# Kernel optimization log

Measured on AMD Instinct MI355X. Metric: run time of the kernel, lower is better.

Reference implementation:

```python
import jax, jax.numpy as jnp
import numpy as np

B, P, N0 = 8, 32, 10000
K, HIDP = 8, 4
HIDR = 4 * K * HIDP + K   # 136 = backbone output channels
HEADS = 2
E = 160000


def _conv_bn(x, w, b, g, be, dil):
    # x: [B,1,P,N0]; w: [k,1,ks,1]; valid conv along time with dilation dil, then BatchNorm2d (batch stats)
    y = jax.lax.conv_general_dilated(x, w, (1, 1), 'VALID', rhs_dilation=(dil, 1),
                                     dimension_numbers=('NCHW', 'OIHW', 'NCHW'))
    y = y + b[None, :, None, None]
    mu = jnp.mean(y, axis=(0, 2, 3), keepdims=True)
    var = jnp.var(y, axis=(0, 2, 3), keepdims=True)
    return g[None, :, None, None] * (y - mu) * jax.lax.rsqrt(var + 1e-5) + be[None, :, None, None]


def _branch(x, w, b, g, be, dil, pool):
    y = _conv_bn(x, w, b, g, be, dil)
    if pool:  # AdaptiveMaxPool2d((HIDP, N0)): pools only the time axis (node axis already N0)
        T = y.shape[2]
        y = jnp.stack([jnp.max(y[:, :, (i * T) // HIDP: -((-(i + 1) * T) // HIDP), :], axis=2)
                       for i in range(HIDP)], axis=2)
    return y.reshape(y.shape[0], -1, y.shape[-1])  # [B, k*hidP or k, N0]


def _backbone(x, pl1, pl2, pp1, pp2, pg):
    x = x.reshape(-1, 1, P, N0)
    parts = [_branch(x, *pl1, 1, True), _branch(x, *pl2, 1, True),   # local: ks 3,5 dil 1
             _branch(x, *pp1, 2, True), _branch(x, *pp2, 2, True),   # periodic: ks 3,5 dil 2
             _branch(x, *pg, 1, False)]                               # global: ks P, no pool
    return jnp.tanh(jnp.concatenate(parts, axis=1).transpose(0, 2, 1))  # [B, N0, HIDR]


def _gat(xn, W, a_src, a_dst, bias, src, dst, heads, out_ch):
    # PyG GATConv: linear (no bias) -> per-head additive attention -> segment softmax over dst -> scatter-sum
    n = xn.shape[0]
    h = (xn @ W).reshape(n, heads, out_ch)                              # [N,H,C]
    al = jax.nn.leaky_relu(jnp.sum(h * a_src, -1)[src] + jnp.sum(h * a_dst, -1)[dst], 0.2)  # [E',H]
    amax = jax.ops.segment_max(al, dst, num_segments=n)
    ex = jnp.exp(al - amax[dst])
    coef = ex / (jax.ops.segment_sum(ex, dst, num_segments=n)[dst] + 1e-16)
    out = jax.ops.segment_sum(coef[:, :, None] * h[src], dst, num_segments=n)  # [N,H,C]
    return out.reshape(n, heads * out_ch) + bias


def setup_inputs() -> dict:
    key = jax.random.key(0)
    ks = iter(jax.random.split(key, 64))
    nrm = lambda *s: jax.random.normal(next(ks), s, jnp.float32) * 0.05
    d = {"x": jax.random.normal(next(ks), (B, P, N0), jnp.float32)}
    for nm, ksz in (("l1", 3), ("l2", 5), ("p1", 3), ("p2", 5), ("g", P)):
        d["w_" + nm] = nrm(K, 1, ksz, 1)
        d["b_" + nm] = nrm(K)
        d["g_" + nm] = jnp.ones((K,), jnp.float32)
        d["be_" + nm] = jnp.zeros((K,), jnp.float32)
    d["W1"] = nrm(HIDR, HEADS * HIDR); d["as1"] = nrm(HEADS, HIDR); d["ad1"] = nrm(HEADS, HIDR); d["bb1"] = nrm(HEADS * HIDR)
    d["W2"] = nrm(HEADS * HIDR, HIDR); d["as2"] = nrm(1, HIDR); d["ad2"] = nrm(1, HIDR); d["bb2"] = nrm(HIDR)
    d["Wo"] = nrm(2 * HIDR, HIDR); d["bo"] = nrm(HIDR)
    d["Wo2"] = nrm(HIDR, 1); d["bo2"] = nrm(1)
    d["edge_index"] = jax.random.randint(next(ks), (2, E), 0, N0, jnp.int32)
    return d


def reference(x, w_l1, b_l1, g_l1, be_l1, w_l2, b_l2, g_l2, be_l2,
              w_p1, b_p1, g_p1, be_p1, w_p2, b_p2, g_p2, be_p2,
              w_g, b_g, g_g, be_g,
              W1, as1, ad1, bb1, W2, as2, ad2, bb2, Wo, bo, Wo2, bo2, edge_index):
    feat = _backbone(x, (w_l1, b_l1, g_l1, be_l1), (w_l2, b_l2, g_l2, be_l2),
                     (w_p1, b_p1, g_p1, be_p1), (w_p2, b_p2, g_p2, be_p2),
                     (w_g, b_g, g_g, be_g))                                  # [B,N0,HIDR]
    loop = jnp.arange(N0, dtype=edge_index.dtype)                            # GATConv add_self_loops=True
    src = jnp.concatenate([edge_index[0], loop])
    dst = jnp.concatenate([edge_index[1], loop])
    # original loops GATConv per batch item over shared edge_index; vmap is the batched equivalent
    g1 = jax.vmap(lambda f: _gat(f, W1, as1, ad1, bb1, src, dst, HEADS, HIDR))(feat)  # [B,N0,2*HIDR]
    g2 = jax.vmap(lambda f: _gat(f, W2, as2, ad2, bb2, src, dst, 1, HIDR))(g1)        # [B,N0,HIDR]
    ns = jax.nn.leaky_relu(jnp.concatenate([g2, feat], axis=-1))             # dropout is identity at eval
    res = jax.nn.leaky_relu(ns @ Wo + bo)
    return (res @ Wo2 + bo2)[..., 0]                                         # [B,N0]
```

## Files before the change

kernel.cpp:

```cpp
#include <hip/hip_runtime.h>
#include <hip/hip_bf16.h>
#include <math.h>

typedef unsigned short u16;
typedef unsigned int   u32;
typedef short v8s __attribute__((ext_vector_type(8)));
typedef float v4f __attribute__((ext_vector_type(4)));
typedef float v2f __attribute__((ext_vector_type(2)));
#define DEV static __device__ __forceinline__

DEV float u2f(u16 u){ union{u32 i; float f;} v; v.i = ((u32)u)<<16; return v.f; }
DEV u16   f2u(float f){ union{float ff; u32 i;} v; v.ff = f; u32 r = v.i + 0x7fffu + ((v.i>>16)&1u); return (u16)(r>>16); }
DEV float lrelu02(float x){ return x > 0.f ? x : 0.2f*x; }
DEV float lrelu01(float x){ return x > 0.f ? x : 0.01f*x; }
DEV float fast_tanh(float x){
  float cx = fminf(fmaxf(x, -15.f), 15.f);
  float e = __expf(2.f*cx);
  return (e - 1.f) * __builtin_amdgcn_rcpf(e + 1.f);
}
DEV float wred_sum(float v){
  #pragma unroll
  for (int o = 32; o > 0; o >>= 1) v += __shfl_xor(v, o, 64);
  return v;
}
DEV float wred_max32(float v){
  #pragma unroll
  for (int o = 16; o > 0; o >>= 1) v = fmaxf(v, __shfl_xor(v, o, 64));
  return v;
}
DEV float wred_sum32(float v){
  #pragma unroll
  for (int o = 16; o > 0; o >>= 1) v += __shfl_xor(v, o, 64);
  return v;
}
DEV v2f unpack2(u32 w){
  v2f r;
  r.x = __uint_as_float(w << 16);
  r.y = __uint_as_float(w & 0xffff0000u);
  return r;
}

constexpr int B_   = 8;
constexpr int P_   = 32;
constexpr int N0_  = 10000;
constexpr int NODES = B_ * N0_;
constexpr int E_   = 160000;
constexpr int NE_  = E_ + N0_;

DEV void load_convw(float* lw, const float* wl1, const float* wl2, const float* wp1,
                    const float* wp2, const float* wg, int tid, int nth){
  for (int i = tid; i < 384; i += nth){
    float v;
    if      (i < 24)  v = wl1[i];
    else if (i < 64)  v = wl2[i-24];
    else if (i < 88)  v = wp1[i-64];
    else if (i < 128) v = wp2[i-88];
    else              v = wg [i-128];
    lw[i] = v;
  }
}

template<int KS,int DIL,int T>
DEV void conv_stats(const float* xc, const float* wk, float& s, float& q){
  #pragma unroll
  for (int t = 0; t < T; t++){
    float v = 0.f;
    #pragma unroll
    for (int j = 0; j < KS; j++) v = fmaf(wk[j], xc[t + j*DIL], v);
    s += v; q = fmaf(v, v, q);
  }
}

__global__ void __launch_bounds__(256) k_mega1(
    const float* __restrict__ Wo, u16* __restrict__ WoT,
    const float* __restrict__ W1, const float* __restrict__ W2, u16* __restrict__ W12T,
    const float* __restrict__ as1, const float* __restrict__ ad1,
    float* __restrict__ va1s, float* __restrict__ va1d,
    const float* __restrict__ as2, const float* __restrict__ ad2,
    const float* __restrict__ bb1,
    float* __restrict__ v2ss, float* __restrict__ v2dd,
    float* __restrict__ cc, float* __restrict__ b12,
    const float* __restrict__ x,
    const float* __restrict__ wl1, const float* __restrict__ wl2,
    const float* __restrict__ wp1, const float* __restrict__ wp2,
    const float* __restrict__ wg,
    float* __restrict__ gsum, float* __restrict__ gsq,
    const int* __restrict__ ei, int* __restrict__ counts)
{
  __shared__ float smem[544];
  int blk = blockIdx.x, tid = threadIdx.x;
  if (blk < 180){
    int i = blk*256 + tid; if (i >= 144*320) return;
    int n = i/320, k = i - n*320; float v = 0.f;
    if (n < 136){
      if (k < 136) v = Wo[(size_t)k*136 + n];
      else if (k >= 160 && k < 296) v = Wo[(size_t)(k-24)*136 + n];
    }
    WoT[i] = f2u(v); return;
  }
  blk -= 180;
  if (blk < 162){
    int i = blk*256 + tid; if (i >= 144*288) return;
    int n = i/288, kk = i - n*288; float v = 0.f;
    if (n < 136 && kk < 272){
      int hh = kk/136, k = kk - hh*136;
      for (int c = 0; c < 136; c++)
        v = fmaf(W1[(size_t)k*272 + hh*136 + c], W2[(size_t)(hh*136+c)*136 + n], v);
    }
    W12T[i] = f2u(v); return;
  }
  blk -= 162;
  if (blk < 2){
    int t = blk*256 + tid; if (t >= 272) return;
    int hh = t/136, k = t - hh*136; float s = 0.f, d = 0.f;
    for (int c = 0; c < 136; c++){
      float w = W1[(size_t)k*272 + hh*136 + c];
      s = fmaf(w, as1[hh*136+c], s);
      d = fmaf(w, ad1[hh*136+c], d);
    }
    va1s[t] = s; va1d[t] = d; return;
  }
  blk -= 2;
  if (blk < 2){
    float* l2s = smem; float* l2d = smem + 272;
    for (int m = tid; m < 272; m += 256){
      float vs = 0.f, vd = 0.f;
      for (int n2 = 0; n2 < 136; n2++){
        float w2 = W2[(size_t)m*136 + n2];
        vs = fmaf(w2, as2[n2], vs);
        vd = fmaf(w2, ad2[n2], vd);
      }
      l2s[m] = vs; l2d[m] = vd;
    }
    __syncthreads();
    int t0 = blk*256 + tid;
    if (t0 < 272){
      int hh = t0/136, k = t0 - hh*136; float s = 0.f, d = 0.f;
      for (int c = 0; c < 136; c++){
        float w = W1[(size_t)k*272 + hh*136 + c];
        s = fmaf(w, l2s[hh*136+c], s);
        d = fmaf(w, l2d[hh*136+c], d);
      }
      v2ss[t0] = s; v2dd[t0] = d;
    }
    if (blk == 1){
      if (tid < 64){
        float s = 0.f, d = 0.f;
        for (int m = tid; m < 272; m += 64){
          s = fmaf(bb1[m], l2s[m], s);
          d = fmaf(bb1[m], l2d[m], d);
        }
        s = wred_sum(s); d = wred_sum(d);
        if (tid == 0){ cc[0] = s; cc[1] = d; }
      } else if (tid < 200){
        int n2 = tid - 64; float v = 0.f;
        for (int m = 0; m < 272; m++) v = fmaf(bb1[m], W2[(size_t)m*136 + n2], v);
        b12[n2] = v;
      }
    }
    return;
  }
  blk -= 2;
  if (blk < 625){
    float* lw = smem; float* lacc = smem + 384;
    load_convw(lw, wl1, wl2, wp1, wp2, wg, tid, 256);
    if (tid < 80) lacc[tid] = 0.f;
    __syncthreads();

    const int lane = tid & 63, wv = tid >> 6;
    const int nodeLocal = (wv >> 1)*64 + lane;
    const int half = wv & 1;
    const int gid = blk*128 + nodeLocal;
    float xc[P_];
    if (gid < NODES){
      int b = gid / N0_, n = gid - b*N0_;
      const float* xp = x + (size_t)b*P_*N0_ + n;
      #pragma unroll
      for (int p = 0; p < P_; p++) xc[p] = xp[(size_t)p*N0_];
    } else {
      #pragma unroll
      for (int p = 0; p < P_; p++) xc[p] = 0.f;
    }

    auto red = [&](int ch, float s, float q){
      #pragma unroll
      for (int o = 32; o > 0; o >>= 1){ s += __shfl_down(s,o,64); q += __shfl_down(q,o,64); }
      if (lane == 0){ atomicAdd(&lacc[ch], s); atomicAdd(&lacc[40+ch], q); }
    };

    if (half == 0){
      #pragma unroll
      for (int k = 0; k < 8; k++){ float s=0,q=0; conv_stats<3,1,30>(xc, lw      + k*3 , s,q); red(k,     s,q); }
      #pragma unroll
      for (int k = 0; k < 8; k++){ float s=0,q=0; conv_stats<5,1,28>(xc, lw + 24 + k*5 , s,q); red(8+k,   s,q); }
    } else {
      #pragma unroll
      for (int k = 0; k < 8; k++){ float s=0,q=0; conv_stats<3,2,28>(xc, lw + 64 + k*3 , s,q); red(16+k,  s,q); }
      #pragma unroll
      for (int k = 0; k < 8; k++){ float s=0,q=0; conv_stats<5,2,24>(xc, lw + 88 + k*5 , s,q); red(24+k,  s,q); }
      #pragma unroll
      for (int k = 0; k < 8; k++){ float s=0,q=0; conv_stats<32,1,1>(xc, lw + 128+ k*32, s,q); red(32+k,  s,q); }
    }

    __syncthreads();
    if (tid < 40)      atomicAdd(&gsum[tid],    lacc[tid]);
    else if (tid < 80) atomicAdd(&gsq [tid-40], lacc[tid]);
    return;
  }
  blk -= 625;
  {
    int e = blk*256 + tid;
    if (e >= NE_) return;
    int dst = (e < E_) ? ei[E_ + e] : (e - E_);
    atomicAdd(&counts[dst], 1);
  }
}

__global__ void __launch_bounds__(1024) k_mega2(
    const int* __restrict__ counts, int* __restrict__ offs, int* __restrict__ perm,
    const float* __restrict__ gsum, const float* __restrict__ gsq,
    float* __restrict__ sA, float* __restrict__ sB,
    const float* g0, const float* g1, const float* g2, const float* g3, const float* g4,
    const float* e0, const float* e1, const float* e2, const float* e3, const float* e4)
{
  __shared__ int part[1024];
  __shared__ int hist[129];
  __shared__ int base[129];
  int t = threadIdx.x;
  if (blockIdx.x == 0){
    if (t >= 40) return;
    int bi = t >> 3, k = t & 7;
    const int Ts[5] = {30,28,28,24,1};
    float cnt  = (float)NODES * (float)Ts[bi];
    float mean = gsum[t] / cnt;
    float var  = gsq[t] / cnt - mean*mean;
    const float* gp = bi==0?g0: bi==1?g1: bi==2?g2: bi==3?g3: g4;
    const float* ep = bi==0?e0: bi==1?e1: bi==2?e2: bi==3?e3: e4;
    float a = gp[k] * rsqrtf(fmaxf(var, 0.f) + 1e-5f);
    sA[t] = a;
    sB[t] = ep[k] - a*mean;
    return;
  }
  if (blockIdx.x == 1){
    int loc[10]; int s = 0;
    #pragma unroll
    for (int i = 0; i < 10; i++){
      int idx = t*10 + i;
      int c = (idx < N0_) ? counts[idx] : 0;
      loc[i] = s; s += c;
    }
    part[t] = s;
    __syncthreads();
    for (int o = 1; o < 1024; o <<= 1){
      int v = (t >= o) ? part[t-o] : 0;
      __syncthreads();
      part[t] += v;
      __syncthreads();
    }
    int pre = (t == 0) ? 0 : part[t-1];
    #pragma unroll
    for (int i = 0; i < 10; i++){
      int idx = t*10 + i;
      if (idx < N0_) offs[idx] = pre + loc[i];
    }
    if (t == 0) offs[N0_] = part[1023];
  } else {
    if (t < 129) hist[t] = 0;
    __syncthreads();
    int dloc[10];
    #pragma unroll
    for (int i = 0; i < 10; i++){
      int idx = t*10 + i;
      if (idx < N0_){
        int d = min(counts[idx], 128);
        dloc[i] = d;
        atomicAdd(&hist[d], 1);
      }
    }
    __syncthreads();
    if (t == 0){
      int s = 0;
      for (int b = 0; b <= 128; b++){ base[b] = s; s += hist[b]; }
    }
    __syncthreads();
    #pragma unroll
    for (int i = 0; i < 10; i++){
      int idx = t*10 + i;
      if (idx < N0_){
        int pos = atomicAdd(&base[dloc[i]], 1);
        perm[pos] = idx;
      }
    }
  }
}

template<int KS,int DIL,int T>
DEV void conv_pool4(const float* xc, const float* wk, float A, float Bc, float* o4){
  float y[T];
  #pragma unroll
  for (int t = 0; t < T; t++){
    float v = 0.f;
    #pragma unroll
    for (int j = 0; j < KS; j++) v = fmaf(wk[j], xc[t + j*DIL], v);
    y[t] = fmaf(A, v, Bc);
  }
  #pragma unroll
  for (int i = 0; i < 4; i++){
    const int lo = (i*T)/4, hi = ((i+1)*T + 3)/4;
    float m = y[lo];
    #pragma unroll
    for (int t = 0; t < T; t++){ if (t > lo && t < hi) m = fmaxf(m, y[t]); }
    o4[i] = m;
  }
}

__global__ void __launch_bounds__(256) k_feat_sc(
    const float* __restrict__ x,
    const float* __restrict__ wl1, const float* __restrict__ wl2,
    const float* __restrict__ wp1, const float* __restrict__ wp2,
    const float* __restrict__ wg,
    const float* __restrict__ sA, const float* __restrict__ sB,
    const float* __restrict__ va1s, const float* __restrict__ va1d,
    u16* __restrict__ feat,
    float* __restrict__ asrc1, float* __restrict__ adst1,
    int base, int m, int featBlocks,
    const int* __restrict__ ei, const int* __restrict__ offs,
    int* __restrict__ cursor, int* __restrict__ srcl)
{
  __shared__ float lw[384];
  __shared__ float lA[40], lB[40];
  __shared__ float4 lv4[136];
  __shared__ float sdt[128][4];
  if (blockIdx.x >= featBlocks){
    int e = (blockIdx.x - featBlocks)*256 + threadIdx.x;
    if (e >= NE_) return;
    int src, dst;
    if (e < E_){ src = ei[e]; dst = ei[E_ + e]; } else { src = dst = e - E_; }
    int pos = atomicAdd(&cursor[dst], 1);
    srcl[offs[dst] + pos] = src;
    return;
  }
  const int tid = threadIdx.x;
  load_convw(lw, wl1, wl2, wp1, wp2, wg, tid, 256);
  if (tid < 40){ lA[tid] = sA[tid]; lB[tid] = sB[tid]; }
  for (int i = tid; i < 136; i += 256)
    lv4[i] = make_float4(va1s[i], va1d[i], va1s[136+i], va1d[136+i]);
  __syncthreads();

  const int lane = tid & 63, wv = tid >> 6;
  const int nodeLocal = (wv >> 1)*64 + lane;
  const int half = wv & 1;
  const int nodeIdx = blockIdx.x*128 + nodeLocal;
  const bool act = nodeIdx < m;
  const int gcl = base + (act ? nodeIdx : (m-1));
  int b = gcl / N0_, n = gcl - b*N0_;
  float xc[P_];
  const float* xp = x + (size_t)b*P_*N0_ + n;
  #pragma unroll
  for (int p = 0; p < P_; p++) xc[p] = xp[(size_t)p*N0_];

  float dt[4] = {0.f,0.f,0.f,0.f};
  u32 pk[4];
  u16* orow  = feat + (size_t)nodeIdx*160;
  auto emit = [&](int ch, float v){
    float t = fast_tanh(v);
    float4 vv = lv4[ch];
    dt[0] = fmaf(t, vv.x, dt[0]);
    dt[1] = fmaf(t, vv.y, dt[1]);
    dt[2] = fmaf(t, vv.z, dt[2]);
    dt[3] = fmaf(t, vv.w, dt[3]);
    u16 h  = f2u(t);
    int s = ch & 7;
    if ((s & 1) == 0){ pk[s>>1] = h; }
    else             { pk[s>>1] |= ((u32)h) << 16; }
    if (s == 7 && act){
      *(uint4*)(orow + (ch - 7)) = make_uint4(pk[0],pk[1],pk[2],pk[3]);
    }
  };

  float o4[4];
  if (half == 0){
    #pragma unroll
    for (int k = 0; k < 8; k++){
      conv_pool4<3,1,30>(xc, lw + k*3, lA[k], lB[k], o4);
      #pragma unroll
      for (int i = 0; i < 4; i++) emit(k*4+i, o4[i]);
    }
    #pragma unroll
    for (int k = 0; k < 8; k++){
      conv_pool4<5,1,28>(xc, lw + 24 + k*5, lA[8+k], lB[8+k], o4);
      #pragma unroll
      for (int i = 0; i < 4; i++) emit(32 + k*4+i, o4[i]);
    }
  } else {
    #pragma unroll
    for (int k = 0; k < 8; k++){
      conv_pool4<3,2,28>(xc, lw + 64 + k*3, lA[16+k], lB[16+k], o4);
      #pragma unroll
      for (int i = 0; i < 4; i++) emit(64 + k*4+i, o4[i]);
    }
    #pragma unroll
    for (int k = 0; k < 8; k++){
      conv_pool4<5,2,24>(xc, lw + 88 + k*5, lA[24+k], lB[24+k], o4);
      #pragma unroll
      for (int i = 0; i < 4; i++) emit(96 + k*4+i, o4[i]);
    }
    #pragma unroll
    for (int k = 0; k < 8; k++){
      float v = 0.f;
      #pragma unroll
      for (int j = 0; j < 32; j++) v = fmaf(lw[128 + k*32 + j], xc[j], v);
      emit(128 + k, fmaf(lA[32+k], v, lB[32+k]));
    }
  }

  if (half == 1){
    sdt[nodeLocal][0] = dt[0]; sdt[nodeLocal][1] = dt[1];
    sdt[nodeLocal][2] = dt[2]; sdt[nodeLocal][3] = dt[3];
  }
  __syncthreads();
  if (half == 0 && act){
    asrc1[(size_t)nodeIdx*2]   = dt[0] + sdt[nodeLocal][0];
    asrc1[(size_t)nodeIdx*2+1] = dt[2] + sdt[nodeLocal][2];
    adst1[(size_t)nodeIdx*2]   = dt[1] + sdt[nodeLocal][1];
    adst1[(size_t)nodeIdx*2+1] = dt[3] + sdt[nodeLocal][3];
  }
}

template<int MT,int KT1,int KT2,int NT,int EPI,int LR2>
__global__ void __launch_bounds__(256) k_mfma(
    const u16* __restrict__ A1, int sA1,
    const u16* __restrict__ A2, int sA2,
    const u16* __restrict__ BT, int sBT,
    u16* __restrict__ C, int sC, int nbase,
    const float* __restrict__ bias, int m,
    const float* __restrict__ w2v, const float* __restrict__ bo2p, float* __restrict__ fout)
{
  const int wv = threadIdx.x >> 6, lane = threadIdx.x & 63;
  const int quad = lane >> 4, l15 = lane & 15;
  const int mb = blockIdx.x*(MT*64) + wv*(MT*16);
  int ar[MT];
  #pragma unroll
  for (int mt = 0; mt < MT; mt++) ar[mt] = min(mb + mt*16 + l15, m-1);

  v4f acc[MT][NT];
  #pragma unroll
  for (int mt = 0; mt < MT; mt++)
    #pragma unroll
    for (int nt = 0; nt < NT; nt++)
      acc[mt][nt] = (v4f){0.f,0.f,0.f,0.f};

  for (int kt = 0; kt < KT1+KT2; kt++){
    const u16* ab; int sA, koff;
    if (KT2 == 0 || kt < KT1){ ab = A1; sA = sA1; koff = kt*32; }
    else { ab = A2; sA = sA2; koff = (kt-KT1)*32; }
    v8s a[MT];
    #pragma unroll
    for (int mt = 0; mt < MT; mt++)
      a[mt] = *(const v8s*)(ab + (size_t)ar[mt]*sA + koff + quad*8);
    if (KT2 > 0 && LR2 && kt >= KT1){
      #pragma unroll
      for (int mt = 0; mt < MT; mt++)
        #pragma unroll
        for (int j = 0; j < 8; j++){
          float f = u2f((u16)a[mt][j]);
          f = f > 0.f ? f : 0.01f*f;
          a[mt][j] = (short)f2u(f);
        }
    }
    const int kb = kt*32 + quad*8;
    #pragma unroll
    for (int nt = 0; nt < NT; nt++){
      v8s b = *(const v8s*)(BT + (size_t)(nbase + nt*16 + l15)*sBT + kb);
      #pragma unroll
      for (int mt = 0; mt < MT; mt++)
        acc[mt][nt] = __builtin_amdgcn_mfma_f32_16x16x32_bf16(a[mt], b, acc[mt][nt], 0, 0, 0);
    }
  }

  if (EPI == 2){
    const float bo2v = bo2p[0];
    #pragma unroll
    for (int mt = 0; mt < MT; mt++){
      float part[4] = {0.f,0.f,0.f,0.f};
      #pragma unroll
      for (int nt = 0; nt < NT; nt++){
        const int col = nt*16 + l15;
        float wv2 = (col < 136) ? w2v[col] : 0.f;
        float bv  = bias[min(col,135)];
        #pragma unroll
        for (int i = 0; i < 4; i++){
          float xv = lrelu01(acc[mt][nt][i] + bv);
          part[i] = fmaf(xv, wv2, part[i]);
        }
      }
      #pragma unroll
      for (int i = 0; i < 4; i++){
        float v = part[i];
        v += __shfl_xor(v, 1, 64);
        v += __shfl_xor(v, 2, 64);
        v += __shfl_xor(v, 4, 64);
        v += __shfl_xor(v, 8, 64);
        int r = mb + mt*16 + quad*4 + i;
        if (l15 == 0 && r < m) fout[r] = v + bo2v;
      }
    }
    return;
  }

  #pragma unroll
  for (int mt = 0; mt < MT; mt++){
    const int r0 = mb + mt*16 + quad*4;
    #pragma unroll
    for (int nt = 0; nt < NT; nt++){
      const int col = nbase + nt*16 + l15;
      #pragma unroll
      for (int i = 0; i < 4; i++){
        int r = r0 + i;
        if (r < m){
          float xv = acc[mt][nt][i];
          if (EPI == 1){ xv += bias[min(col,135)]; xv = lrelu01(xv); }
          if (EPI == 3){ xv += bias[min(col,135)]; }
          C[(size_t)r*sC + col] = f2u(xv);
        }
      }
    }
  }
}

__global__ void __launch_bounds__(256) k_agg1(const u16* __restrict__ feat,
    const float* __restrict__ asrc, const float* __restrict__ adst,
    const int* __restrict__ offs, const int* __restrict__ srcl,
    const int* __restrict__ perm,
    u16* __restrict__ aggF,
    const float* __restrict__ v2s, const float* __restrict__ v2d,
    const float* __restrict__ cc,
    float* __restrict__ as_out, float* __restrict__ ad_out,
    int cbMask, int cbShift)
{
  __shared__ int4 smeta[4][2][32];
  const int tid = threadIdx.x;
  const int wv = tid >> 6, lane = tid & 63;
  const int half = lane >> 5, l32 = lane & 31;
  const int id = blockIdx.x;
  const int bb = id & cbMask;
  const int q = (id >> cbShift)*4 + wv;
  const int dst = perm[N0_ - 1 - 2*q - half];
  const int nbase = bb*N0_;
  const int node = nbase + dst;
  const int start = offs[dst], end = offs[dst+1];
  const int ne = end - start;

  const float ad0 = adst[(size_t)node*2], ad1v = adst[(size_t)node*2+1];
  const char* featB = (const char*)feat;

  v2f m01h0 = {0.f,0.f}, m23h0 = {0.f,0.f};
  v2f m01h1 = {0.f,0.f}, m23h1 = {0.f,0.f};
  v2f r01h0 = {0.f,0.f}, r01h1 = {0.f,0.f};

  auto acc_one = [&](int4 mt){
    const u16* fp = (const u16*)(featB + mt.x);
    float c0 = __int_as_float(mt.y), c1 = __int_as_float(mt.z);
    const uint2 hv = *(const uint2*)(fp + 4*l32);
    v2f f01 = unpack2(hv.x), f23 = unpack2(hv.y);
    v2f cc0 = {c0,c0}, cc1 = {c1,c1};
    m01h0 = __builtin_elementwise_fma(f01, cc0, m01h0);
    m23h0 = __builtin_elementwise_fma(f23, cc0, m23h0);
    m01h1 = __builtin_elementwise_fma(f01, cc1, m01h1);
    m23h1 = __builtin_elementwise_fma(f23, cc1, m23h1);
    if (l32 < 4){
      const u32 hr = *(const u32*)(fp + 128 + 2*l32);
      v2f g01 = unpack2(hr);
      r01h0 = __builtin_elementwise_fma(g01, cc0, r01h0);
      r01h1 = __builtin_elementwise_fma(g01, cc1, r01h1);
    }
  };
  auto acc_four = [&](int4 ma, int4 mb, int4 mc, int4 md){
    const u16* p0 = (const u16*)(featB + ma.x);
    const u16* p1 = (const u16*)(featB + mb.x);
    const u16* p2 = (const u16*)(featB + mc.x);
    const u16* p3 = (const u16*)(featB + md.x);
    const uint2 v0 = *(const uint2*)(p0 + 4*l32);
    const uint2 v1 = *(const uint2*)(p1 + 4*l32);
    const uint2 v2 = *(const uint2*)(p2 + 4*l32);
    const uint2 v3 = *(const uint2*)(p3 + 4*l32);
    u32 q0, q1, q2, q3;
    if (l32 < 4){
      q0 = *(const u32*)(p0 + 128 + 2*l32);
      q1 = *(const u32*)(p1 + 128 + 2*l32);
      q2 = *(const u32*)(p2 + 128 + 2*l32);
      q3 = *(const u32*)(p3 + 128 + 2*l32);
    }
    v2f f01, f23, cA, cB;
    #define EDGE1(vv, qq, mm) \
      f01 = unpack2(vv.x); f23 = unpack2(vv.y); \
      cA = (v2f){__int_as_float(mm.y), __int_as_float(mm.y)}; \
      cB = (v2f){__int_as_float(mm.z), __int_as_float(mm.z)}; \
      m01h0 = __builtin_elementwise_fma(f01, cA, m01h0); \
      m23h0 = __builtin_elementwise_fma(f23, cA, m23h0); \
      m01h1 = __builtin_elementwise_fma(f01, cB, m01h1); \
      m23h1 = __builtin_elementwise_fma(f23, cB, m23h1); \
      if (l32 < 4){ \
        v2f g01 = unpack2(qq); \
        r01h0 = __builtin_elementwise_fma(g01, cA, r01h0); \
        r01h1 = __builtin_elementwise_fma(g01, cB, r01h1); \
      }
    EDGE1(v0, q0, ma)
    EDGE1(v1, q1, mb)
    EDGE1(v2, q2, mc)
    EDGE1(v3, q3, md)
    #undef EDGE1
  };
  auto run_chunk = [&](int cnt){
    const int4* mp = &smeta[wv][half][0];
    int j = 0;
    for (; j + 3 < cnt; j += 4)
      acc_four(mp[j], mp[j+1], mp[j+2], mp[j+3]);
    for (; j < cnt; j++)
      acc_one(mp[j]);
  };

  if (ne <= 32){
    const bool has = l32 < ne;
    const int sn = nbase + (has ? srcl[start + l32] : 0);
    const int offL = sn * 320;
    float al0 = has ? lrelu02(asrc[(size_t)sn*2]   + ad0)  : -1e30f;
    float al1 = has ? lrelu02(asrc[(size_t)sn*2+1] + ad1v) : -1e30f;
    float mm = wred_max32(al0);
    float p0 = has ? __expf(al0 - mm) : 0.f;
    float c0 = p0 * (1.f/(wred_sum32(p0) + 1e-16f));
    mm = wred_max32(al1);
    float p1 = has ? __expf(al1 - mm) : 0.f;
    float c1 = p1 * (1.f/(wred_sum32(p1) + 1e-16f));
    if (has)
      smeta[wv][half][l32] = make_int4(offL, __float_as_int(c0), __float_as_int(c1), 0);
    asm volatile("s_waitcnt lgkmcnt(0)" ::: "memory");
    run_chunk(ne);
  } else {
    float lm0 = -1e30f, lm1 = -1e30f;
    for (int e = start + l32; e < end; e += 32){
      int sn = nbase + srcl[e];
      lm0 = fmaxf(lm0, lrelu02(asrc[(size_t)sn*2]   + ad0));
      lm1 = fmaxf(lm1, lrelu02(asrc[(size_t)sn*2+1] + ad1v));
    }
    float m0 = wred_max32(lm0), m1 = wred_max32(lm1);
    float ls0 = 0.f, ls1 = 0.f;
    for (int e = start + l32; e < end; e += 32){
      int sn = nbase + srcl[e];
      ls0 += __expf(lrelu02(asrc[(size_t)sn*2]   + ad0)  - m0);
      ls1 += __expf(lrelu02(asrc[(size_t)sn*2+1] + ad1v) - m1);
    }
    float si0 = 1.f/(wred_sum32(ls0) + 1e-16f);
    float si1 = 1.f/(wred_sum32(ls1) + 1e-16f);
    for (int cs = start; cs < end; cs += 32){
      int cnt = min(32, end - cs);
      bool has = l32 < cnt;
      int sn = nbase + (has ? srcl[cs + l32] : 0);
      int offL = sn * 320;
      float c0 = 0.f, c1 = 0.f;
      if (has){
        c0 = __expf(lrelu02(asrc[(size_t)sn*2]   + ad0)  - m0) * si0;
        c1 = __expf(lrelu02(asrc[(size_t)sn*2+1] + ad1v) - m1) * si1;
      }
      if (has)
        smeta[wv][half][l32] = make_int4(offL, __float_as_int(c0), __float_as_int(c1), 0);
      asm volatile("s_waitcnt lgkmcnt(0)" ::: "memory");
      run_chunk(cnt);
    }
  }

  u16* outp = aggF + (size_t)node*288;
  {
    ushort4 s0; s0.x=f2u(m01h0.x); s0.y=f2u(m01h0.y); s0.z=f2u(m23h0.x); s0.w=f2u(m23h0.y);
    *(ushort4*)(outp + 4*l32) = s0;
    ushort4 s1; s1.x=f2u(m01h1.x); s1.y=f2u(m01h1.y); s1.z=f2u(m23h1.x); s1.w=f2u(m23h1.y);
    *(ushort4*)(outp + 136 + 4*l32) = s1;
    if (l32 < 4){
      ushort2 t0; t0.x=f2u(r01h0.x); t0.y=f2u(r01h0.y);
      *(ushort2*)(outp + 128 + 2*l32) = t0;
      ushort2 t1; t1.x=f2u(r01h1.x); t1.y=f2u(r01h1.y);
      *(ushort2*)(outp + 136 + 128 + 2*l32) = t1;
    }
  }
  {
    int c = 4*l32;
    float s = m01h0.x*v2s[c] + m01h0.y*v2s[c+1] + m23h0.x*v2s[c+2] + m23h0.y*v2s[c+3]
            + m01h1.x*v2s[136+c] + m01h1.y*v2s[136+c+1] + m23h1.x*v2s[136+c+2] + m23h1.y*v2s[136+c+3];
    float d = m01h0.x*v2d[c] + m01h0.y*v2d[c+1] + m23h0.x*v2d[c+2] + m23h0.y*v2d[c+3]
            + m01h1.x*v2d[136+c] + m01h1.y*v2d[136+c+1] + m23h1.x*v2d[136+c+2] + m23h1.y*v2d[136+c+3];
    if (l32 < 4){
      int cr = 128 + 2*l32;
      s += r01h0.x*v2s[cr] + r01h0.y*v2s[cr+1] + r01h1.x*v2s[136+cr] + r01h1.y*v2s[136+cr+1];
      d += r01h0.x*v2d[cr] + r01h0.y*v2d[cr+1] + r01h1.x*v2d[136+cr] + r01h1.y*v2d[136+cr+1];
    }
    s = wred_sum32(s); d = wred_sum32(d);
    if (l32 == 0){ as_out[node] = s + cc[0]; ad_out[node] = d + cc[1]; }
  }
}

__global__ void __launch_bounds__(256) k_agg2(const u16* __restrict__ h, int sh,
    const float* __restrict__ asrc, const float* __restrict__ adst,
    const int* __restrict__ offs, const int* __restrict__ srcl,
    const int* __restrict__ perm,
    const float* __restrict__ bias, u16* __restrict__ outp0, int so,
    int cbMask, int cbShift)
{
  __shared__ int2 smeta[4][2][32];
  const int tid = threadIdx.x;
  const int wv = tid >> 6, lane = tid & 63;
  const int half = lane >> 5, l32 = lane & 31;
  const int id = blockIdx.x;
  const int bb = id & cbMask;
  const int q = (id >> cbShift)*4 + wv;
  const int dst = perm[N0_ - 1 - 2*q - half];
  const int nbase = bb*N0_;
  const int node = nbase + dst;
  const int start = offs[dst], end = offs[dst+1];
  const int ne = end - start;
  const int bstride = 2*sh;

  const float adh = adst[node];
  const char* hB = (const char*)h;

  v2f a01 = {0.f,0.f}, a23 = {0.f,0.f}, r01 = {0.f,0.f};

  auto acc_one = [&](int2 mt){
    const u16* hp = (const u16*)(hB + mt.x);
    float c0 = __int_as_float(mt.y);
    const uint2 hv = *(const uint2*)(hp + 4*l32);
    v2f cc0 = {c0,c0};
    a01 = __builtin_elementwise_fma(unpack2(hv.x), cc0, a01);
    a23 = __builtin_elementwise_fma(unpack2(hv.y), cc0, a23);
    if (l32 < 4){
      const u32 hr = *(const u32*)(hp + 128 + 2*l32);
      r01 = __builtin_elementwise_fma(unpack2(hr), cc0, r01);
    }
  };
  auto acc_four = [&](int2 ma, int2 mb, int2 mc, int2 md){
    const u16* p0 = (const u16*)(hB + ma.x);
    const u16* p1 = (const u16*)(hB + mb.x);
    const u16* p2 = (const u16*)(hB + mc.x);
    const u16* p3 = (const u16*)(hB + md.x);
    const uint2 v0 = *(const uint2*)(p0 + 4*l32);
    const uint2 v1 = *(const uint2*)(p1 + 4*l32);
    const uint2 v2 = *(const uint2*)(p2 + 4*l32);
    const uint2 v3 = *(const uint2*)(p3 + 4*l32);
    u32 q0, q1, q2, q3;
    if (l32 < 4){
      q0 = *(const u32*)(p0 + 128 + 2*l32);
      q1 = *(const u32*)(p1 + 128 + 2*l32);
      q2 = *(const u32*)(p2 + 128 + 2*l32);
      q3 = *(const u32*)(p3 + 128 + 2*l32);
    }
    v2f cc;
    #define EDGE2(vv, qq, mm) \
      cc = (v2f){__int_as_float(mm.y), __int_as_float(mm.y)}; \
      a01 = __builtin_elementwise_fma(unpack2(vv.x), cc, a01); \
      a23 = __builtin_elementwise_fma(unpack2(vv.y), cc, a23); \
      if (l32 < 4) r01 = __builtin_elementwise_fma(unpack2(qq), cc, r01);
    EDGE2(v0, q0, ma)
    EDGE2(v1, q1, mb)
    EDGE2(v2, q2, mc)
    EDGE2(v3, q3, md)
    #undef EDGE2
  };
  auto run_chunk = [&](int cnt){
    const int2* mp = &smeta[wv][half][0];
    int j = 0;
    for (; j + 3 < cnt; j += 4)
      acc_four(mp[j], mp[j+1], mp[j+2], mp[j+3]);
    for (; j < cnt; j++)
      acc_one(mp[j]);
  };

  if (ne <= 32){
    const bool has = l32 < ne;
    const int sn = nbase + (has ? srcl[start + l32] : 0);
    const int offL = sn * bstride;
    float al = has ? lrelu02(asrc[sn] + adh) : -1e30f;
    float m = wred_max32(al);
    float p = has ? __expf(al - m) : 0.f;
    float c0 = p * (1.f/(wred_sum32(p) + 1e-16f));
    if (has)
      smeta[wv][half][l32] = make_int2(offL, __float_as_int(c0));
    asm volatile("s_waitcnt lgkmcnt(0)" ::: "memory");
    run_chunk(ne);
  } else {
    float lm = -1e30f;
    for (int e = start + l32; e < end; e += 32){
      int sn = nbase + srcl[e];
      lm = fmaxf(lm, lrelu02(asrc[sn] + adh));
    }
    float m = wred_max32(lm);
    float ls = 0.f;
    for (int e = start + l32; e < end; e += 32){
      int sn = nbase + srcl[e];
      ls += __expf(lrelu02(asrc[sn] + adh) - m);
    }
    float si = 1.f/(wred_sum32(ls) + 1e-16f);
    for (int cs = start; cs < end; cs += 32){
      int cnt = min(32, end - cs);
      bool has = l32 < cnt;
      int sn = nbase + (has ? srcl[cs + l32] : 0);
      int offL = sn * bstride;
      float c0 = has ? __expf(lrelu02(asrc[sn] + adh) - m) * si : 0.f;
      if (has)
        smeta[wv][half][l32] = make_int2(offL, __float_as_int(c0));
      asm volatile("s_waitcnt lgkmcnt(0)" ::: "memory");
      run_chunk(cnt);
    }
  }

  u16* outp = outp0 + (size_t)node*so;
  {
    int c = 4*l32;
    ushort4 st;
    st.x = f2u(lrelu01(a01.x + bias[c]));
    st.y = f2u(lrelu01(a01.y + bias[c+1]));
    st.z = f2u(lrelu01(a23.x + bias[c+2]));
    st.w = f2u(lrelu01(a23.y + bias[c+3]));
    *(ushort4*)(outp + c) = st;
    if (l32 < 4){
      int cr = 128 + 2*l32;
      ushort2 sr;
      sr.x = f2u(lrelu01(r01.x + bias[cr]));
      sr.y = f2u(lrelu01(r01.y + bias[cr+1]));
      *(ushort2*)(outp + cr) = sr;
    }
  }
}

extern "C" void kernel_launch(void* const* d_in, const int* in_sizes, int n_in,
                              void* d_out, int out_size, void* d_ws, size_t ws_size,
                              hipStream_t stream)
{
  (void)in_sizes; (void)n_in; (void)out_size;
  const float* x    = (const float*)d_in[0];
  const float* wl1  = (const float*)d_in[1];
  const float* gl1  = (const float*)d_in[3];
  const float* bel1 = (const float*)d_in[4];
  const float* wl2  = (const float*)d_in[5];
  const float* gl2  = (const float*)d_in[7];
  const float* bel2 = (const float*)d_in[8];
  const float* wp1  = (const float*)d_in[9];
  const float* gp1  = (const float*)d_in[11];
  const float* bep1 = (const float*)d_in[12];
  const float* wp2  = (const float*)d_in[13];
  const float* gp2  = (const float*)d_in[15];
  const float* bep2 = (const float*)d_in[16];
  const float* wg   = (const float*)d_in[17];
  const float* gg   = (const float*)d_in[19];
  const float* beg  = (const float*)d_in[20];
  const float* W1   = (const float*)d_in[21];
  const float* as1  = (const float*)d_in[22];
  const float* ad1  = (const float*)d_in[23];
  const float* bb1  = (const float*)d_in[24];
  const float* W2   = (const float*)d_in[25];
  const float* as2  = (const float*)d_in[26];
  const float* ad2  = (const float*)d_in[27];
  const float* bb2  = (const float*)d_in[28];
  const float* Wo   = (const float*)d_in[29];
  const float* bo   = (const float*)d_in[30];
  const float* Wo2  = (const float*)d_in[31];
  const float* bo2  = (const float*)d_in[32];
  const int*   ei   = (const int*)d_in[33];

  const size_t STATIC_BYTES = 1250000;
  int nc = 1;
  while (nc < 8 && STATIC_BYTES + (size_t)1560*(NODES/nc) > ws_size) nc <<= 1;
  const int CB = B_/nc, CN = CB*N0_;
  int cbShift = 0; while ((1 << cbShift) < CB) cbShift++;
  const int cbMask = CB - 1;

  char* wsb = (char*)d_ws; size_t off = 0;
  auto alloc = [&](size_t nbytes)->void*{
    void* p = wsb + off; off = (off + nbytes + 255) & ~(size_t)255; return p;
  };
  int*   zbase  = (int*)  alloc(20080*sizeof(int));
  float* gsum   = (float*)zbase;
  float* gsq    = gsum + 40;
  int*   counts = zbase + 80;
  int*   cursor = counts + 10000;
  float* sA     = (float*)alloc(40*sizeof(float));
  float* sB     = (float*)alloc(40*sizeof(float));
  int*   offs   = (int*)  alloc(10001*sizeof(int));
  int*   srcl   = (int*)  alloc((size_t)NE_*sizeof(int));
  int*   perm   = (int*)  alloc((size_t)N0_*sizeof(int));
  u16*   W12T   = (u16*)  alloc((size_t)144*288*2);
  u16*   WoT    = (u16*)  alloc((size_t)144*320*2);
  float* va1s   = (float*)alloc(272*sizeof(float));
  float* va1d   = (float*)alloc(272*sizeof(float));
  float* v2ss   = (float*)alloc(272*sizeof(float));
  float* v2dd   = (float*)alloc(272*sizeof(float));
  float* ccv    = (float*)alloc(2*sizeof(float));
  float* b12    = (float*)alloc(136*sizeof(float));
  u16*   feat   = (u16*)  alloc((size_t)CN*160*2);
  u16*   aggF   = (u16*)  alloc((size_t)CN*288*2);
  u16*   h2     = (u16*)  alloc((size_t)CN*144*2);
  u16*   g2l    = (u16*)  alloc((size_t)CN*160*2);
  float* asrc1  = (float*)alloc((size_t)CN*2*sizeof(float));
  float* adst1  = (float*)alloc((size_t)CN*2*sizeof(float));
  float* asrc2  = (float*)alloc((size_t)CN*sizeof(float));
  float* adst2  = (float*)alloc((size_t)CN*sizeof(float));

  hipMemsetAsync(zbase, 0, 20080*sizeof(int), stream);

  k_mega1<<<1636,256,0,stream>>>(Wo, WoT, W1, W2, W12T,
                                 as1, ad1, va1s, va1d, as2, ad2, bb1,
                                 v2ss, v2dd, ccv, b12,
                                 x, wl1, wl2, wp1, wp2, wg, gsum, gsq,
                                 ei, counts);

  k_mega2<<<3,1024,0,stream>>>(counts, offs, perm, gsum, gsq, sA, sB,
                               gl1,gl2,gp1,gp2,gg, bel1,bel2,bep1,bep2,beg);

  const int gxm = (CN + 127)/128;
  const int gx2 = (CN + 127)/128;
  const int aggB = 1250*CB;
  for (int c = 0; c < nc; c++){
    const int base = c*CN;

    const int extra = (c == 0) ? 665 : 0;
    k_feat_sc<<<gx2 + extra,256,0,stream>>>(x, wl1,wl2,wp1,wp2,wg, sA, sB, va1s, va1d,
                                            feat, asrc1, adst1, base, CN, gx2,
                                            ei, offs, cursor, srcl);

    k_agg1<<<aggB,256,0,stream>>>(feat, asrc1, adst1, offs, srcl, perm, aggF,
                                  v2ss, v2dd, ccv, asrc2, adst2, cbMask, cbShift);

    k_mfma<2,9,0,9,3,0><<<gxm,256,0,stream>>>(aggF,288, (const u16*)0,0, W12T,288, h2,144, 0, b12, CN,
                                              (const float*)0,(const float*)0,(float*)0);

    k_agg2<<<aggB,256,0,stream>>>(h2,144, asrc2, adst2, offs, srcl, perm, bb2, g2l,160,
                                  cbMask, cbShift);

    k_mfma<2,5,5,9,2,1><<<gxm,256,0,stream>>>(g2l,160, feat,160, WoT,320, (u16*)0,0, 0, bo, CN,
                                              Wo2, bo2, (float*)d_out + base);
  }
}
```

Before: 412.8 us.

## Precompute layer-2 attention projections per source node in feature kernel

The layer-2 attention scalars were computed after aggregation by dotting the aggregated features with the folded weight vectors. They are now projected per node in the feature kernel, using linearity: a dot of aggregated features equals the coefficient-weighted sum of per-source dots. These per-node values are packed with the layer-1 scores into an 8-float record. The aggregation kernel then accumulates scalar sums instead of doing a wide reduction over channels. This costs extra FMAs and a larger per-node metadata read per edge.

```diff
diff --git a/kernel.cpp b/kernel.cpp
--- a/kernel.cpp
+++ b/kernel.cpp
@@ -321,8 +321,9 @@
     const float* __restrict__ wg,
     const float* __restrict__ sA, const float* __restrict__ sB,
     const float* __restrict__ va1s, const float* __restrict__ va1d,
+    const float* __restrict__ v2ss, const float* __restrict__ v2dd,
     u16* __restrict__ feat,
-    float* __restrict__ asrc1, float* __restrict__ adst1,
+    float* __restrict__ nodeMeta,
     int base, int m, int featBlocks,
     const int* __restrict__ ei, const int* __restrict__ offs,
     int* __restrict__ cursor, int* __restrict__ srcl)
@@ -330,7 +331,8 @@
   __shared__ float lw[384];
   __shared__ float lA[40], lB[40];
   __shared__ float4 lv4[136];
-  __shared__ float sdt[128][4];
+  __shared__ float4 lvv[136];
+  __shared__ float sdt[128][8];
   if (blockIdx.x >= featBlocks){
     int e = (blockIdx.x - featBlocks)*256 + threadIdx.x;
     if (e >= NE_) return;
@@ -343,8 +345,10 @@
   const int tid = threadIdx.x;
   load_convw(lw, wl1, wl2, wp1, wp2, wg, tid, 256);
   if (tid < 40){ lA[tid] = sA[tid]; lB[tid] = sB[tid]; }
-  for (int i = tid; i < 136; i += 256)
+  for (int i = tid; i < 136; i += 256){
     lv4[i] = make_float4(va1s[i], va1d[i], va1s[136+i], va1d[136+i]);
+    lvv[i] = make_float4(v2ss[i], v2dd[i], v2ss[136+i], v2dd[136+i]);
+  }
   __syncthreads();
 
   const int lane = tid & 63, wv = tid >> 6;
@@ -359,7 +363,7 @@
   #pragma unroll
   for (int p = 0; p < P_; p++) xc[p] = xp[(size_t)p*N0_];
 
-  float dt[4] = {0.f,0.f,0.f,0.f};
+  float dt[8] = {0.f,0.f,0.f,0.f,0.f,0.f,0.f,0.f};
   u32 pk[4];
   u16* orow  = feat + (size_t)nodeIdx*160;
   auto emit = [&](int ch, float v){
@@ -369,6 +373,11 @@
     dt[1] = fmaf(t, vv.y, dt[1]);
     dt[2] = fmaf(t, vv.z, dt[2]);
     dt[3] = fmaf(t, vv.w, dt[3]);
+    float4 w2 = lvv[ch];
+    dt[4] = fmaf(t, w2.x, dt[4]);
+    dt[5] = fmaf(t, w2.y, dt[5]);
+    dt[6] = fmaf(t, w2.z, dt[6]);
+    dt[7] = fmaf(t, w2.w, dt[7]);
     u16 h  = f2u(t);
     int s = ch & 7;
     if ((s & 1) == 0){ pk[s>>1] = h; }
@@ -415,15 +424,23 @@
   }
 
   if (half == 1){
-    sdt[nodeLocal][0] = dt[0]; sdt[nodeLocal][1] = dt[1];
-    sdt[nodeLocal][2] = dt[2]; sdt[nodeLocal][3] = dt[3];
+    #pragma unroll
+    for (int i = 0; i < 8; i++) sdt[nodeLocal][i] = dt[i];
   }
   __syncthreads();
   if (half == 0 && act){
-    asrc1[(size_t)nodeIdx*2]   = dt[0] + sdt[nodeLocal][0];
-    asrc1[(size_t)nodeIdx*2+1] = dt[2] + sdt[nodeLocal][2];
-    adst1[(size_t)nodeIdx*2]   = dt[1] + sdt[nodeLocal][1];
-    adst1[(size_t)nodeIdx*2+1] = dt[3] + sdt[nodeLocal][3];
+    float* mp = nodeMeta + (size_t)nodeIdx*8;
+    float4 m0, m1;
+    m0.x = dt[0] + sdt[nodeLocal][0];
+    m0.y = dt[2] + sdt[nodeLocal][2];
+    m0.z = dt[4] + sdt[nodeLocal][4];
+    m0.w = dt[6] + sdt[nodeLocal][6];
+    m1.x = dt[5] + sdt[nodeLocal][5];
+    m1.y = dt[7] + sdt[nodeLocal][7];
+    m1.z = dt[1] + sdt[nodeLocal][1];
+    m1.w = dt[3] + sdt[nodeLocal][3];
+    *(float4*)(mp)     = m0;
+    *(float4*)(mp + 4) = m1;
   }
 }
 
@@ -529,11 +546,10 @@
 }
 
 __global__ void __launch_bounds__(256) k_agg1(const u16* __restrict__ feat,
-    const float* __restrict__ asrc, const float* __restrict__ adst,
+    const float* __restrict__ meta,
     const int* __restrict__ offs, const int* __restrict__ srcl,
     const int* __restrict__ perm,
     u16* __restrict__ aggF,
-    const float* __restrict__ v2s, const float* __restrict__ v2d,
     const float* __restrict__ cc,
     float* __restrict__ as_out, float* __restrict__ ad_out,
     int cbMask, int cbShift)
@@ -551,12 +567,13 @@
   const int start = offs[dst], end = offs[dst+1];
   const int ne = end - start;
 
-  const float ad0 = adst[(size_t)node*2], ad1v = adst[(size_t)node*2+1];
+  const float2 adv = *(const float2*)(meta + (size_t)node*8 + 6);
   const char* featB = (const char*)feat;
 
   v2f m01h0 = {0.f,0.f}, m23h0 = {0.f,0.f};
   v2f m01h1 = {0.f,0.f}, m23h1 = {0.f,0.f};
   v2f r01h0 = {0.f,0.f}, r01h1 = {0.f,0.f};
+  float sAcc = 0.f, dAcc = 0.f;
 
   auto acc_one = [&](int4 mt){
     const u16* fp = (const u16*)(featB + mt.x);
@@ -624,14 +641,22 @@
     const bool has = l32 < ne;
     const int sn = nbase + (has ? srcl[start + l32] : 0);
     const int offL = sn * 320;
-    float al0 = has ? lrelu02(asrc[(size_t)sn*2]   + ad0)  : -1e30f;
-    float al1 = has ? lrelu02(asrc[(size_t)sn*2+1] + ad1v) : -1e30f;
+    float4 MA = make_float4(0.f,0.f,0.f,0.f);
+    float2 MD = make_float2(0.f,0.f);
+    if (has){
+      MA = *(const float4*)(meta + (size_t)sn*8);
+      MD = *(const float2*)(meta + (size_t)sn*8 + 4);
+    }
+    float al0 = has ? lrelu02(MA.x + adv.x) : -1e30f;
+    float al1 = has ? lrelu02(MA.y + adv.y) : -1e30f;
     float mm = wred_max32(al0);
     float p0 = has ? __expf(al0 - mm) : 0.f;
     float c0 = p0 * (1.f/(wred_sum32(p0) + 1e-16f));
     mm = wred_max32(al1);
     float p1 = has ? __expf(al1 - mm) : 0.f;
     float c1 = p1 * (1.f/(wred_sum32(p1) + 1e-16f));
+    sAcc = c0*MA.z + c1*MA.w;
+    dAcc = c0*MD.x + c1*MD.y;
     if (has)
       smeta[wv][half][l32] = make_int4(offL, __float_as_int(c0), __float_as_int(c1), 0);
     asm volatile("s_waitcnt lgkmcnt(0)" ::: "memory");
@@ -640,15 +665,17 @@
     float lm0 = -1e30f, lm1 = -1e30f;
     for (int e = start + l32; e < end; e += 32){
       int sn = nbase + srcl[e];
-      lm0 = fmaxf(lm0, lrelu02(asrc[(size_t)sn*2]   + ad0));
-      lm1 = fmaxf(lm1, lrelu02(asrc[(size_t)sn*2+1] + ad1v));
+      float2 AS = *(const float2*)(meta + (size_t)sn*8);
+      lm0 = fmaxf(lm0, lrelu02(AS.x + adv.x));
+      lm1 = fmaxf(lm1, lrelu02(AS.y + adv.y));
     }
     float m0 = wred_max32(lm0), m1 = wred_max32(lm1);
     float ls0 = 0.f, ls1 = 0.f;
     for (int e = start + l32; e < end; e += 32){
       int sn = nbase + srcl[e];
-      ls0 += __expf(lrelu02(asrc[(size_t)sn*2]   + ad0)  - m0);
-      ls1 += __expf(lrelu02(asrc[(size_t)sn*2+1] + ad1v) - m1);
+      float2 AS = *(const float2*)(meta + (size_t)sn*8);
+      ls0 += __expf(lrelu02(AS.x + adv.x) - m0);
+      ls1 += __expf(lrelu02(AS.y + adv.y) - m1);
     }
     float si0 = 1.f/(wred_sum32(ls0) + 1e-16f);
     float si1 = 1.f/(wred_sum32(ls1) + 1e-16f);
@@ -659,8 +686,12 @@
       int offL = sn * 320;
       float c0 = 0.f, c1 = 0.f;
       if (has){
-        c0 = __expf(lrelu02(asrc[(size_t)sn*2]   + ad0)  - m0) * si0;
-        c1 = __expf(lrelu02(asrc[(size_t)sn*2+1] + ad1v) - m1) * si1;
+        float4 MA = *(const float4*)(meta + (size_t)sn*8);
+        float2 MD = *(const float2*)(meta + (size_t)sn*8 + 4);
+        c0 = __expf(lrelu02(MA.x + adv.x) - m0) * si0;
+        c1 = __expf(lrelu02(MA.y + adv.y) - m1) * si1;
+        sAcc = fmaf(c0, MA.z, fmaf(c1, MA.w, sAcc));
+        dAcc = fmaf(c0, MD.x, fmaf(c1, MD.y, dAcc));
       }
       if (has)
         smeta[wv][half][l32] = make_int4(offL, __float_as_int(c0), __float_as_int(c1), 0);
@@ -682,20 +713,9 @@
       *(ushort2*)(outp + 136 + 128 + 2*l32) = t1;
     }
   }
-  {
-    int c = 4*l32;
-    float s = m01h0.x*v2s[c] + m01h0.y*v2s[c+1] + m23h0.x*v2s[c+2] + m23h0.y*v2s[c+3]
-            + m01h1.x*v2s[136+c] + m01h1.y*v2s[136+c+1] + m23h1.x*v2s[136+c+2] + m23h1.y*v2s[136+c+3];
-    float d = m01h0.x*v2d[c] + m01h0.y*v2d[c+1] + m23h0.x*v2d[c+2] + m23h0.y*v2d[c+3]
-            + m01h1.x*v2d[136+c] + m01h1.y*v2d[136+c+1] + m23h1.x*v2d[136+c+2] + m23h1.y*v2d[136+c+3];
-    if (l32 < 4){
-      int cr = 128 + 2*l32;
-      s += r01h0.x*v2s[cr] + r01h0.y*v2s[cr+1] + r01h1.x*v2s[136+cr] + r01h1.y*v2s[136+cr+1];
-      d += r01h0.x*v2d[cr] + r01h0.y*v2d[cr+1] + r01h1.x*v2d[136+cr] + r01h1.y*v2d[136+cr+1];
-    }
-    s = wred_sum32(s); d = wred_sum32(d);
-    if (l32 == 0){ as_out[node] = s + cc[0]; ad_out[node] = d + cc[1]; }
-  }
+  sAcc = wred_sum32(sAcc);
+  dAcc = wred_sum32(dAcc);
+  if (l32 == 0){ as_out[node] = sAcc + cc[0]; ad_out[node] = dAcc + cc[1]; }
 }
 
 __global__ void __launch_bounds__(256) k_agg2(const u16* __restrict__ h, int sh,
@@ -867,7 +887,7 @@
 
   const size_t STATIC_BYTES = 1250000;
   int nc = 1;
-  while (nc < 8 && STATIC_BYTES + (size_t)1560*(NODES/nc) > ws_size) nc <<= 1;
+  while (nc < 8 && STATIC_BYTES + (size_t)1600*(NODES/nc) > ws_size) nc <<= 1;
   const int CB = B_/nc, CN = CB*N0_;
   int cbShift = 0; while ((1 << cbShift) < CB) cbShift++;
   const int cbMask = CB - 1;
@@ -898,8 +918,7 @@
   u16*   aggF   = (u16*)  alloc((size_t)CN*288*2);
   u16*   h2     = (u16*)  alloc((size_t)CN*144*2);
   u16*   g2l    = (u16*)  alloc((size_t)CN*160*2);
-  float* asrc1  = (float*)alloc((size_t)CN*2*sizeof(float));
-  float* adst1  = (float*)alloc((size_t)CN*2*sizeof(float));
+  float* nodeMeta = (float*)alloc((size_t)CN*8*sizeof(float));
   float* asrc2  = (float*)alloc((size_t)CN*sizeof(float));
   float* adst2  = (float*)alloc((size_t)CN*sizeof(float));
 
@@ -922,11 +941,12 @@
 
     const int extra = (c == 0) ? 665 : 0;
     k_feat_sc<<<gx2 + extra,256,0,stream>>>(x, wl1,wl2,wp1,wp2,wg, sA, sB, va1s, va1d,
-                                            feat, asrc1, adst1, base, CN, gx2,
+                                            v2ss, v2dd,
+                                            feat, nodeMeta, base, CN, gx2,
                                             ei, offs, cursor, srcl);
 
-    k_agg1<<<aggB,256,0,stream>>>(feat, asrc1, adst1, offs, srcl, perm, aggF,
-                                  v2ss, v2dd, ccv, asrc2, adst2, cbMask, cbShift);
+    k_agg1<<<aggB,256,0,stream>>>(feat, nodeMeta, offs, srcl, perm, aggF,
+                                  ccv, asrc2, adst2, cbMask, cbShift);
 
     k_mfma<2,9,0,9,3,0><<<gxm,256,0,stream>>>(aggF,288, (const u16*)0,0, W12T,288, h2,144, 0, b12, CN,
                                               (const float*)0,(const float*)0,(float*)0);
```

Result: slower. 462.0 us (+11.9%).
